# Kernel optimization log

Hardware: AMD Instinct MI355X
Metric: run time of the kernel (lower is better)

## Reference

```python
import jax, jax.numpy as jnp
import numpy as np

B, S, H, I, E, TOPK = 2, 2048, 1024, 2048, 8, 2


def setup_inputs() -> dict:
    key = jax.random.key(0)
    k0, k1, k2, k3, k4 = jax.random.split(key, 5)
    return {
        "hidden_state": jax.random.normal(k0, (B, S, H), dtype=jnp.float32),
        "gate_w": jax.random.normal(k1, (H, E), dtype=jnp.float32) * 0.02,
        "Wg": jax.random.normal(k2, (E, H, I), dtype=jnp.float32) * 0.02,
        "Wu": jax.random.normal(k3, (E, H, I), dtype=jnp.float32) * 0.02,
        "Wd": jax.random.normal(k4, (E, I, H), dtype=jnp.float32) * 0.02,
        "top_k": TOPK,
    }


def reference(hidden_state, gate_w, Wg, Wu, Wd, top_k):
    b, s, h = hidden_state.shape
    x = hidden_state.reshape(-1, h)                      # [T, H]
    T = x.shape[0]
    router_logits = x @ gate_w                           # [T, E]
    probs = jax.nn.softmax(router_logits, axis=-1)
    top_p, top_i = jax.lax.top_k(probs, top_k)           # [T, K]
    # norm_expert=False -> no renormalization of top-k probs
    # scatter top-k probs into dense per-expert combine weights [T, E]
    weights = jnp.zeros((T, probs.shape[-1]), dtype=x.dtype)
    weights = weights.at[jnp.arange(T)[:, None], top_i].add(top_p)
    # dense per-expert SwiGLU MLP (equivalent math to gather/scatter dispatch)
    g = jnp.einsum('th,ehi->tei', x, Wg)                 # [T, E, I]
    u = jnp.einsum('th,ehi->tei', x, Wu)
    mid = jax.nn.silu(g) * u
    expert_out = jnp.einsum('tei,eih->teh', mid, Wd)     # [T, E, H]
    final = jnp.einsum('te,teh->th', weights, expert_out)
    return final.reshape(b, s, h), router_logits
```

## Files before the change

### kernel.cpp

```cpp
#include <hip/hip_runtime.h>
#include <stdint.h>
#include <math.h>

#define T_TOK 4096
#define H_DIM 1024
#define I_DIM 2048
#define E_NUM 8
#define PMAX (T_TOK * 2 + E_NUM * 128)

#define WCONV_BLOCKS (E_NUM * 512 * 3)
#define ROUTER_BLOCKS (T_TOK / 4)

typedef __attribute__((ext_vector_type(8))) short short8;
typedef __attribute__((ext_vector_type(4))) float f32x4;
typedef unsigned short u16;
typedef unsigned int u32;

__device__ __forceinline__ u16 f2bf(float f) {
  union { float f; u32 u; } v; v.f = f;
  u32 r = v.u + 0x7fffu + ((v.u >> 16) & 1u);
  return (u16)(r >> 16);
}
__device__ __forceinline__ float bf2f(u16 a) {
  union { u32 u; float f; } v; v.u = ((u32)a) << 16; return v.f;
}

__device__ __forceinline__ void async_ld16(const u16* g, u16* l) {
  __builtin_amdgcn_global_load_lds(
      (const __attribute__((address_space(1))) void*)g,
      (__attribute__((address_space(3))) void*)l, 16, 0, 0);
}

__global__ void front_kernel(const float* __restrict__ Wg, const float* __restrict__ Wu,
                             const float* __restrict__ Wd, u16* __restrict__ wgt,
                             u16* __restrict__ wut, u16* __restrict__ wdt,
                             const float* __restrict__ x, u16* __restrict__ xb,
                             const float* __restrict__ gw, float* __restrict__ logits_out,
                             int* __restrict__ te, float* __restrict__ tw) {
  __shared__ float sgw[E_NUM * H_DIM];
  const int b = blockIdx.x;
  if (b < WCONV_BLOCKS) {
    const int zz = b / (E_NUM * 512);
    const int idx = b - zz * (E_NUM * 512);
    const float* src = (zz == 0) ? Wg : (zz == 1) ? Wu : Wd;
    u16* dst = (zz == 0) ? wgt : (zz == 1) ? wut : wdt;
    const int R = (zz == 2) ? I_DIM : H_DIM;
    const int C = (zz == 2) ? H_DIM : I_DIM;
    const int cpt = C >> 6;
    const int e = idx >> 9;
    const int ti = idx & 511;
    const int r0 = (ti / cpt) << 6;
    const int c0 = (ti % cpt) << 6;
    const float* s = src + (size_t)e * H_DIM * I_DIM;
    u16* d = dst + (size_t)e * H_DIM * I_DIM;

    const int wave = threadIdx.x >> 6, lane = threadIdx.x & 63;
    const int g = lane >> 4, lq = lane & 15;
    const int c = c0 + wave * 16 + g * 4;
    const int r = r0 + lq * 4;

    float4 v0 = *(const float4*)(s + (size_t)(r + 0) * C + c);
    float4 v1 = *(const float4*)(s + (size_t)(r + 1) * C + c);
    float4 v2 = *(const float4*)(s + (size_t)(r + 2) * C + c);
    float4 v3 = *(const float4*)(s + (size_t)(r + 3) * C + c);

    ushort4 o;
    o.x = f2bf(v0.x); o.y = f2bf(v1.x); o.z = f2bf(v2.x); o.w = f2bf(v3.x);
    *(ushort4*)(d + (size_t)(c + 0) * R + r) = o;
    o.x = f2bf(v0.y); o.y = f2bf(v1.y); o.z = f2bf(v2.y); o.w = f2bf(v3.y);
    *(ushort4*)(d + (size_t)(c + 1) * R + r) = o;
    o.x = f2bf(v0.z); o.y = f2bf(v1.z); o.z = f2bf(v2.z); o.w = f2bf(v3.z);
    *(ushort4*)(d + (size_t)(c + 2) * R + r) = o;
    o.x = f2bf(v0.w); o.y = f2bf(v1.w); o.z = f2bf(v2.w); o.w = f2bf(v3.w);
    *(ushort4*)(d + (size_t)(c + 3) * R + r) = o;
  } else {
    const int rb = b - WCONV_BLOCKS;
    for (int j = threadIdx.x; j < (H_DIM * E_NUM) / 4; j += 256) {
      float4 v = ((const float4*)gw)[j];
      int base = j * 4;
      sgw[((base + 0) & 7) * H_DIM + ((base + 0) >> 3)] = v.x;
      sgw[((base + 1) & 7) * H_DIM + ((base + 1) >> 3)] = v.y;
      sgw[((base + 2) & 7) * H_DIM + ((base + 2) >> 3)] = v.z;
      sgw[((base + 3) & 7) * H_DIM + ((base + 3) >> 3)] = v.w;
    }
    __syncthreads();
    const int wave = threadIdx.x >> 6, lane = threadIdx.x & 63;
    const int t = rb * 4 + wave;
    const float* xr = x + (size_t)t * H_DIM;
    u16* xbr = xb + (size_t)t * H_DIM;
    float acc[8];
#pragma unroll
    for (int e = 0; e < 8; e++) acc[e] = 0.f;
#pragma unroll
    for (int it = 0; it < 4; it++) {
      int h0 = it * 256 + lane * 4;
      float4 xv = *(const float4*)(xr + h0);
      ushort4 o;
      o.x = f2bf(xv.x); o.y = f2bf(xv.y); o.z = f2bf(xv.z); o.w = f2bf(xv.w);
      *(ushort4*)(xbr + h0) = o;
#pragma unroll
      for (int e = 0; e < 8; e++) {
        float4 g = *(const float4*)(&sgw[e * H_DIM + h0]);
        acc[e] += xv.x * g.x + xv.y * g.y + xv.z * g.z + xv.w * g.w;
      }
    }
#pragma unroll
    for (int m = 1; m < 64; m <<= 1) {
#pragma unroll
      for (int e = 0; e < 8; e++) acc[e] += __shfl_xor(acc[e], m, 64);
    }
    if (lane == 0) {
      float mx = acc[0];
#pragma unroll
      for (int e = 1; e < 8; e++) mx = fmaxf(mx, acc[e]);
      float p[8]; float s = 0.f;
#pragma unroll
      for (int e = 0; e < 8; e++) { p[e] = __expf(acc[e] - mx); s += p[e]; }
      float inv = 1.0f / s;
      int e0 = 0; float b0 = acc[0];
#pragma unroll
      for (int e = 1; e < 8; e++) if (acc[e] > b0) { b0 = acc[e]; e0 = e; }
      int e1 = -1; float b1 = -1e30f;
#pragma unroll
      for (int e = 0; e < 8; e++) if (e != e0 && acc[e] > b1) { b1 = acc[e]; e1 = e; }
#pragma unroll
      for (int e = 0; e < 8; e++) logits_out[(size_t)t * 8 + e] = acc[e];
      te[t * 2] = e0; te[t * 2 + 1] = e1;
      tw[t * 2] = p[e0] * inv; tw[t * 2 + 1] = p[e1] * inv;
    }
  }
}

__global__ __launch_bounds__(1024) void sort_kernel(const int* __restrict__ te,
                                                    int* __restrict__ offs,
                                                    int* __restrict__ token_list,
                                                    int* __restrict__ tpos) {
  __shared__ int wsum[16][8];
  __shared__ int wbase[16][8];
  __shared__ int soffs[9];
  const int tid = threadIdx.x;
  const int wave = tid >> 6, lane = tid & 63;

  for (int j = tid; j < PMAX; j += 1024) token_list[j] = 0;

  const int t0 = tid * 4;
  int e_loc[8];
  int cnt[8];
#pragma unroll
  for (int e = 0; e < 8; e++) cnt[e] = 0;
#pragma unroll
  for (int k = 0; k < 8; k++) {
    int e = te[t0 * 2 + k];
    e_loc[k] = e;
    cnt[e]++;
  }
  int excl[8];
#pragma unroll
  for (int e = 0; e < 8; e++) {
    int v = cnt[e];
    int s = v;
#pragma unroll
    for (int d = 1; d < 64; d <<= 1) {
      int u = __shfl_up(s, d, 64);
      if (lane >= d) s += u;
    }
    excl[e] = s - v;
    if (lane == 63) wsum[wave][e] = s;
  }
  __syncthreads();
  if (tid < 8) {
    int e = tid;
    int a = 0;
    for (int w2 = 0; w2 < 16; w2++) { wbase[w2][e] = a; a += wsum[w2][e]; }
    wsum[0][e] = a;
  }
  __syncthreads();
  if (tid == 0) {
    int a = 0;
    for (int e = 0; e < 8; e++) {
      soffs[e] = a;
      a += (wsum[0][e] + 127) & ~127;
    }
    soffs[8] = a;
    for (int e = 0; e <= 8; e++) offs[e] = soffs[e];
  }
  __syncthreads();
  int base[8];
#pragma unroll
  for (int e = 0; e < 8; e++) base[e] = soffs[e] + wbase[wave][e] + excl[e];
#pragma unroll
  for (int k = 0; k < 8; k++) {
    int e = e_loc[k];
    int pos = base[e]++;
    int t = t0 + (k >> 1);
    token_list[pos] = t;
    tpos[t * 2 + (k & 1)] = pos;
  }
}

#define BK1 64

__global__ __launch_bounds__(256, 2) void gemm1_kernel(
    const u16* __restrict__ xb, const u16* __restrict__ wgt, const u16* __restrict__ wut,
    const int* __restrict__ token_list, const int* __restrict__ offs, u16* __restrict__ mid) {
  const int e = blockIdx.z;
  const int off = offs[e];
  const int pcount = offs[e + 1] - off;
  const int row0 = blockIdx.y * 128;
  if (row0 >= pcount) return;
  const int n0 = blockIdx.x * 128;

  __shared__ __align__(16) u16 As[128 * BK1];
  __shared__ __align__(16) u16 Bg[128 * BK1];
  __shared__ __align__(16) u16 Bu[128 * BK1];

  const int tid = threadIdx.x;
  const int wave = tid >> 6, lane = tid & 63;
  const int wm = (wave >> 1) * 64, wn = (wave & 1) * 64;
  const int quad = lane >> 4, lr = lane & 15;
  const int l7 = lr & 7;

  f32x4 accg[4][4], accu[4][4];
  f32x4 z = {0.f, 0.f, 0.f, 0.f};
#pragma unroll
  for (int i = 0; i < 4; i++)
#pragma unroll
    for (int j = 0; j < 4; j++) { accg[i][j] = z; accu[i][j] = z; }

  const u16* wgb = wgt + (size_t)e * I_DIM * H_DIM;
  const u16* wub = wut + (size_t)e * I_DIM * H_DIM;

  const u16* ga[4]; const u16* gg[4]; const u16* gu[4];
  u16 *la[4], *lg[4], *lu[4];
#pragma unroll
  for (int i = 0; i < 4; i++) {
    int c = tid + 256 * i;
    int row = c >> 3, kcl = c & 7;
    int kg = kcl ^ (row & 7);
    int tok = token_list[off + row0 + row];
    ga[i] = xb + (size_t)tok * H_DIM + kg * 8;
    gg[i] = wgb + (size_t)(n0 + row) * H_DIM + kg * 8;
    gu[i] = wub + (size_t)(n0 + row) * H_DIM + kg * 8;
    la[i] = &As[c * 8]; lg[i] = &Bg[c * 8]; lu[i] = &Bu[c * 8];
  }

  for (int kt = 0; kt < H_DIM / BK1; kt++) {
    const int k0 = kt * BK1;
#pragma unroll
    for (int i = 0; i < 4; i++) {
      async_ld16(ga[i] + k0, la[i]);
      async_ld16(gg[i] + k0, lg[i]);
      async_ld16(gu[i] + k0, lu[i]);
    }
    __syncthreads();
#pragma unroll
    for (int kk = 0; kk < 2; kk++) {
      const int slot = ((kk << 2) + quad) ^ l7;
      short8 af[4];
#pragma unroll
      for (int im = 0; im < 4; im++)
        af[im] = *(const short8*)(&As[(wm + im * 16 + lr) * BK1 + slot * 8]);
#pragma unroll
      for (int in = 0; in < 4; in++) {
        short8 bg = *(const short8*)(&Bg[(wn + in * 16 + lr) * BK1 + slot * 8]);
        short8 bu = *(const short8*)(&Bu[(wn + in * 16 + lr) * BK1 + slot * 8]);
#pragma unroll
        for (int im = 0; im < 4; im++) {
          accg[im][in] = __builtin_amdgcn_mfma_f32_16x16x32_bf16(af[im], bg, accg[im][in], 0, 0, 0);
          accu[im][in] = __builtin_amdgcn_mfma_f32_16x16x32_bf16(af[im], bu, accu[im][in], 0, 0, 0);
        }
      }
    }
    __syncthreads();
  }

#pragma unroll
  for (int im = 0; im < 4; im++) {
#pragma unroll
    for (int r = 0; r < 4; r++) {
      int row = row0 + wm + im * 16 + quad * 4 + r;
      u16* mrow = mid + (size_t)(off + row) * I_DIM + n0 + wn;
#pragma unroll
      for (int in = 0; in < 4; in++) {
        float g = accg[im][in][r];
        float u = accu[im][in][r];
        float sv = g / (1.0f + __expf(-g)) * u;
        mrow[in * 16 + lr] = f2bf(sv);
      }
    }
  }
}

__global__ __launch_bounds__(256, 2) void gemm2_kernel(
    const u16* __restrict__ mid, const u16* __restrict__ wdt,
    const int* __restrict__ offs, u16* __restrict__ eout) {
  const int e = blockIdx.z;
  const int off = offs[e];
  const int pcount = offs[e + 1] - off;
  const int row0 = blockIdx.y * 128;
  if (row0 >= pcount) return;
  const int n0 = blockIdx.x * 128;

  __shared__ __align__(16) u16 As[128 * BK1];
  __shared__ __align__(16) u16 Bs[128 * BK1];

  const int tid = threadIdx.x;
  const int wave = tid >> 6, lane = tid & 63;
  const int wm = (wave >> 1) * 64, wn = (wave & 1) * 64;
  const int quad = lane >> 4, lr = lane & 15;
  const int l7 = lr & 7;

  f32x4 acc[4][4];
  f32x4 z = {0.f, 0.f, 0.f, 0.f};
#pragma unroll
  for (int i = 0; i < 4; i++)
#pragma unroll
    for (int j = 0; j < 4; j++) acc[i][j] = z;

  const u16* wdb = wdt + (size_t)e * H_DIM * I_DIM;

  const u16* ga[4]; const u16* gb[4];
  u16 *la[4], *lb[4];
#pragma unroll
  for (int i = 0; i < 4; i++) {
    int c = tid + 256 * i;
    int row = c >> 3, kcl = c & 7;
    int kg = kcl ^ (row & 7);
    ga[i] = mid + (size_t)(off + row0 + row) * I_DIM + kg * 8;
    gb[i] = wdb + (size_t)(n0 + row) * I_DIM + kg * 8;
    la[i] = &As[c * 8]; lb[i] = &Bs[c * 8];
  }

  for (int kt = 0; kt < I_DIM / BK1; kt++) {
    const int k0 = kt * BK1;
#pragma unroll
    for (int i = 0; i < 4; i++) {
      async_ld16(ga[i] + k0, la[i]);
      async_ld16(gb[i] + k0, lb[i]);
    }
    __syncthreads();
#pragma unroll
    for (int kk = 0; kk < 2; kk++) {
      const int slot = ((kk << 2) + quad) ^ l7;
      short8 af[4];
#pragma unroll
      for (int im = 0; im < 4; im++)
        af[im] = *(const short8*)(&As[(wm + im * 16 + lr) * BK1 + slot * 8]);
#pragma unroll
      for (int in = 0; in < 4; in++) {
        short8 bf = *(const short8*)(&Bs[(wn + in * 16 + lr) * BK1 + slot * 8]);
#pragma unroll
        for (int im = 0; im < 4; im++)
          acc[im][in] = __builtin_amdgcn_mfma_f32_16x16x32_bf16(af[im], bf, acc[im][in], 0, 0, 0);
      }
    }
    __syncthreads();
  }

#pragma unroll
  for (int im = 0; im < 4; im++) {
#pragma unroll
    for (int r = 0; r < 4; r++) {
      int row = row0 + wm + im * 16 + quad * 4 + r;
      u16* orow = eout + (size_t)(off + row) * H_DIM + n0 + wn;
#pragma unroll
      for (int in = 0; in < 4; in++)
        orow[in * 16 + lr] = f2bf(acc[im][in][r]);
    }
  }
}

__global__ void combine_kernel(const u16* __restrict__ eout, const int* __restrict__ tpos,
                               const float* __restrict__ tw, float* __restrict__ out) {
  const int half = threadIdx.x >> 7;
  const int t = blockIdx.x * 2 + half;
  const int lt = threadIdx.x & 127;
  const int h0 = lt * 8;
  const int p0 = tpos[t * 2], p1 = tpos[t * 2 + 1];
  const float w0 = tw[t * 2], w1 = tw[t * 2 + 1];
  ushort4 a0 = *(const ushort4*)(eout + (size_t)p0 * H_DIM + h0);
  ushort4 a1 = *(const ushort4*)(eout + (size_t)p0 * H_DIM + h0 + 4);
  ushort4 b0 = *(const ushort4*)(eout + (size_t)p1 * H_DIM + h0);
  ushort4 b1 = *(const ushort4*)(eout + (size_t)p1 * H_DIM + h0 + 4);
  float4 o0, o1;
  o0.x = w0 * bf2f(a0.x) + w1 * bf2f(b0.x);
  o0.y = w0 * bf2f(a0.y) + w1 * bf2f(b0.y);
  o0.z = w0 * bf2f(a0.z) + w1 * bf2f(b0.z);
  o0.w = w0 * bf2f(a0.w) + w1 * bf2f(b0.w);
  o1.x = w0 * bf2f(a1.x) + w1 * bf2f(b1.x);
  o1.y = w0 * bf2f(a1.y) + w1 * bf2f(b1.y);
  o1.z = w0 * bf2f(a1.z) + w1 * bf2f(b1.z);
  o1.w = w0 * bf2f(a1.w) + w1 * bf2f(b1.w);
  float* orow = out + (size_t)t * H_DIM + h0;
  *(float4*)(orow) = o0;
  *(float4*)(orow + 4) = o1;
}

extern "C" void kernel_launch(void* const* d_in, const int* in_sizes, int n_in,
                              void* d_out, int out_size, void* d_ws, size_t ws_size,
                              hipStream_t stream) {
  const float* x  = (const float*)d_in[0];
  const float* gw = (const float*)d_in[1];
  const float* Wg = (const float*)d_in[2];
  const float* Wu = (const float*)d_in[3];
  const float* Wd = (const float*)d_in[4];
  float* out = (float*)d_out;
  float* out_logits = out + (size_t)T_TOK * H_DIM;

  char* w = (char*)d_ws;
  size_t o = 0;
  auto take = [&](size_t bytes) { char* p = w + o; o += (bytes + 255) & ~(size_t)255; return p; };
  int*   offs        = (int*)take((E_NUM + 1) * 4);
  int*   te          = (int*)take((size_t)T_TOK * 2 * 4);
  float* tw          = (float*)take((size_t)T_TOK * 2 * 4);
  int*   token_list  = (int*)take((size_t)PMAX * 4);
  int*   tpos        = (int*)take((size_t)T_TOK * 2 * 4);
  u16*   xb          = (u16*)take((size_t)T_TOK * H_DIM * 2);
  u16*   wgt         = (u16*)take((size_t)E_NUM * H_DIM * I_DIM * 2);
  u16*   wut         = (u16*)take((size_t)E_NUM * H_DIM * I_DIM * 2);
  u16*   wdt         = (u16*)take((size_t)E_NUM * H_DIM * I_DIM * 2);
  u16*   mid         = (u16*)take((size_t)PMAX * I_DIM * 2);
  u16*   eout        = wgt;
  (void)in_sizes; (void)n_in; (void)out_size; (void)ws_size;

  front_kernel<<<WCONV_BLOCKS + ROUTER_BLOCKS, 256, 0, stream>>>(
      Wg, Wu, Wd, wgt, wut, wdt, x, xb, gw, out_logits, te, tw);
  sort_kernel<<<1, 1024, 0, stream>>>(te, offs, token_list, tpos);
  gemm1_kernel<<<dim3(I_DIM / 128, PMAX / 128, E_NUM), 256, 0, stream>>>(xb, wgt, wut, token_list, offs, mid);
  gemm2_kernel<<<dim3(H_DIM / 128, PMAX / 128, E_NUM), 256, 0, stream>>>(mid, wdt, offs, eout);
  combine_kernel<<<T_TOK / 2, 256, 0, stream>>>(eout, tpos, tw, out);
}
```

Measured before the change: 406.3 us.

## Switch expert GEMMs to 32x32x16 MFMA and a flattened padded-row grid

Both grouped GEMM kernels now use the 32x32x16 bf16 MFMA with 2x2 fragments per wave instead of 4x4 fragments of 16x16x32. This halves the LDS fragment reads per MFMA and changes the register layout of the epilogue. The launch grid is flattened from a 3D per-expert grid to a 1D grid over padded global row tiles, with the expert found by scanning the offsets. Far fewer blocks launch only to exit early. The epilogue stores become strided row writes of 32 lanes, which may coalesce less well.

```diff
diff --git a/kernel.cpp b/kernel.cpp
--- a/kernel.cpp
+++ b/kernel.cpp
@@ -12,7 +12,7 @@
 #define ROUTER_BLOCKS (T_TOK / 4)
 
 typedef __attribute__((ext_vector_type(8))) short short8;
-typedef __attribute__((ext_vector_type(4))) float f32x4;
+typedef __attribute__((ext_vector_type(16))) float f32x16;
 typedef unsigned short u16;
 typedef unsigned int u32;
 
@@ -203,12 +203,13 @@
 __global__ __launch_bounds__(256, 2) void gemm1_kernel(
     const u16* __restrict__ xb, const u16* __restrict__ wgt, const u16* __restrict__ wut,
     const int* __restrict__ token_list, const int* __restrict__ offs, u16* __restrict__ mid) {
-  const int e = blockIdx.z;
-  const int off = offs[e];
-  const int pcount = offs[e + 1] - off;
-  const int row0 = blockIdx.y * 128;
-  if (row0 >= pcount) return;
-  const int n0 = blockIdx.x * 128;
+  const int bid = blockIdx.x;
+  const int my = bid >> 4, nx = bid & 15;
+  const int grow0 = my * 128;
+  if (grow0 >= offs[E_NUM]) return;
+  int e = 0;
+  while (offs[e + 1] <= grow0) e++;
+  const int n0 = nx * 128;
 
   __shared__ __align__(16) u16 As[128 * BK1];
   __shared__ __align__(16) u16 Bg[128 * BK1];
@@ -217,15 +218,16 @@
   const int tid = threadIdx.x;
   const int wave = tid >> 6, lane = tid & 63;
   const int wm = (wave >> 1) * 64, wn = (wave & 1) * 64;
-  const int quad = lane >> 4, lr = lane & 15;
-  const int l7 = lr & 7;
-
-  f32x4 accg[4][4], accu[4][4];
-  f32x4 z = {0.f, 0.f, 0.f, 0.f};
-#pragma unroll
-  for (int i = 0; i < 4; i++)
-#pragma unroll
-    for (int j = 0; j < 4; j++) { accg[i][j] = z; accu[i][j] = z; }
+  const int l31 = lane & 31, kh = lane >> 5;
+
+  f32x16 accg[2][2], accu[2][2];
+#pragma unroll
+  for (int i = 0; i < 2; i++)
+#pragma unroll
+    for (int j = 0; j < 2; j++) {
+      accg[i][j] = (f32x16)(0.f);
+      accu[i][j] = (f32x16)(0.f);
+    }
 
   const u16* wgb = wgt + (size_t)e * I_DIM * H_DIM;
   const u16* wub = wut + (size_t)e * I_DIM * H_DIM;
@@ -237,7 +239,7 @@
     int c = tid + 256 * i;
     int row = c >> 3, kcl = c & 7;
     int kg = kcl ^ (row & 7);
-    int tok = token_list[off + row0 + row];
+    int tok = token_list[grow0 + row];
     ga[i] = xb + (size_t)tok * H_DIM + kg * 8;
     gg[i] = wgb + (size_t)(n0 + row) * H_DIM + kg * 8;
     gu[i] = wub + (size_t)(n0 + row) * H_DIM + kg * 8;
@@ -254,52 +256,58 @@
     }
     __syncthreads();
 #pragma unroll
-    for (int kk = 0; kk < 2; kk++) {
-      const int slot = ((kk << 2) + quad) ^ l7;
-      short8 af[4];
-#pragma unroll
-      for (int im = 0; im < 4; im++)
-        af[im] = *(const short8*)(&As[(wm + im * 16 + lr) * BK1 + slot * 8]);
-#pragma unroll
-      for (int in = 0; in < 4; in++) {
-        short8 bg = *(const short8*)(&Bg[(wn + in * 16 + lr) * BK1 + slot * 8]);
-        short8 bu = *(const short8*)(&Bu[(wn + in * 16 + lr) * BK1 + slot * 8]);
-#pragma unroll
-        for (int im = 0; im < 4; im++) {
-          accg[im][in] = __builtin_amdgcn_mfma_f32_16x16x32_bf16(af[im], bg, accg[im][in], 0, 0, 0);
-          accu[im][in] = __builtin_amdgcn_mfma_f32_16x16x32_bf16(af[im], bu, accu[im][in], 0, 0, 0);
+    for (int ks = 0; ks < 4; ks++) {
+      const int lc = ks * 2 + kh;
+      short8 af[2], bgf[2], buf2[2];
+#pragma unroll
+      for (int mb = 0; mb < 2; mb++) {
+        int row = wm + mb * 32 + l31;
+        af[mb] = *(const short8*)(&As[row * BK1 + (lc ^ (row & 7)) * 8]);
+      }
+#pragma unroll
+      for (int nb = 0; nb < 2; nb++) {
+        int row = wn + nb * 32 + l31;
+        int sl = (lc ^ (row & 7)) * 8;
+        bgf[nb] = *(const short8*)(&Bg[row * BK1 + sl]);
+        buf2[nb] = *(const short8*)(&Bu[row * BK1 + sl]);
+      }
+#pragma unroll
+      for (int mb = 0; mb < 2; mb++)
+#pragma unroll
+        for (int nb = 0; nb < 2; nb++) {
+          accg[mb][nb] = __builtin_amdgcn_mfma_f32_32x32x16_bf16(af[mb], bgf[nb], accg[mb][nb], 0, 0, 0);
+          accu[mb][nb] = __builtin_amdgcn_mfma_f32_32x32x16_bf16(af[mb], buf2[nb], accu[mb][nb], 0, 0, 0);
         }
-      }
     }
     __syncthreads();
   }
 
 #pragma unroll
-  for (int im = 0; im < 4; im++) {
-#pragma unroll
-    for (int r = 0; r < 4; r++) {
-      int row = row0 + wm + im * 16 + quad * 4 + r;
-      u16* mrow = mid + (size_t)(off + row) * I_DIM + n0 + wn;
-#pragma unroll
-      for (int in = 0; in < 4; in++) {
-        float g = accg[im][in][r];
-        float u = accu[im][in][r];
+  for (int mb = 0; mb < 2; mb++)
+#pragma unroll
+    for (int nb = 0; nb < 2; nb++) {
+      u16* base = mid + (size_t)(grow0 + wm + mb * 32 + 4 * kh) * I_DIM + n0 + wn + nb * 32 + l31;
+#pragma unroll
+      for (int reg = 0; reg < 16; reg++) {
+        int dr = (reg & 3) + 8 * (reg >> 2);
+        float g = accg[mb][nb][reg];
+        float u = accu[mb][nb][reg];
         float sv = g / (1.0f + __expf(-g)) * u;
-        mrow[in * 16 + lr] = f2bf(sv);
-      }
-    }
-  }
+        base[(size_t)dr * I_DIM] = f2bf(sv);
+      }
+    }
 }
 
 __global__ __launch_bounds__(256, 2) void gemm2_kernel(
     const u16* __restrict__ mid, const u16* __restrict__ wdt,
     const int* __restrict__ offs, u16* __restrict__ eout) {
-  const int e = blockIdx.z;
-  const int off = offs[e];
-  const int pcount = offs[e + 1] - off;
-  const int row0 = blockIdx.y * 128;
-  if (row0 >= pcount) return;
-  const int n0 = blockIdx.x * 128;
+  const int bid = blockIdx.x;
+  const int my = bid >> 3, nx = bid & 7;
+  const int grow0 = my * 128;
+  if (grow0 >= offs[E_NUM]) return;
+  int e = 0;
+  while (offs[e + 1] <= grow0) e++;
+  const int n0 = nx * 128;
 
   __shared__ __align__(16) u16 As[128 * BK1];
   __shared__ __align__(16) u16 Bs[128 * BK1];
@@ -307,15 +315,13 @@
   const int tid = threadIdx.x;
   const int wave = tid >> 6, lane = tid & 63;
   const int wm = (wave >> 1) * 64, wn = (wave & 1) * 64;
-  const int quad = lane >> 4, lr = lane & 15;
-  const int l7 = lr & 7;
-
-  f32x4 acc[4][4];
-  f32x4 z = {0.f, 0.f, 0.f, 0.f};
-#pragma unroll
-  for (int i = 0; i < 4; i++)
-#pragma unroll
-    for (int j = 0; j < 4; j++) acc[i][j] = z;
+  const int l31 = lane & 31, kh = lane >> 5;
+
+  f32x16 acc[2][2];
+#pragma unroll
+  for (int i = 0; i < 2; i++)
+#pragma unroll
+    for (int j = 0; j < 2; j++) acc[i][j] = (f32x16)(0.f);
 
   const u16* wdb = wdt + (size_t)e * H_DIM * I_DIM;
 
@@ -326,7 +332,7 @@
     int c = tid + 256 * i;
     int row = c >> 3, kcl = c & 7;
     int kg = kcl ^ (row & 7);
-    ga[i] = mid + (size_t)(off + row0 + row) * I_DIM + kg * 8;
+    ga[i] = mid + (size_t)(grow0 + row) * I_DIM + kg * 8;
     gb[i] = wdb + (size_t)(n0 + row) * I_DIM + kg * 8;
     la[i] = &As[c * 8]; lb[i] = &Bs[c * 8];
   }
@@ -340,34 +346,39 @@
     }
     __syncthreads();
 #pragma unroll
-    for (int kk = 0; kk < 2; kk++) {
-      const int slot = ((kk << 2) + quad) ^ l7;
-      short8 af[4];
-#pragma unroll
-      for (int im = 0; im < 4; im++)
-        af[im] = *(const short8*)(&As[(wm + im * 16 + lr) * BK1 + slot * 8]);
-#pragma unroll
-      for (int in = 0; in < 4; in++) {
-        short8 bf = *(const short8*)(&Bs[(wn + in * 16 + lr) * BK1 + slot * 8]);
-#pragma unroll
-        for (int im = 0; im < 4; im++)
-          acc[im][in] = __builtin_amdgcn_mfma_f32_16x16x32_bf16(af[im], bf, acc[im][in], 0, 0, 0);
-      }
+    for (int ks = 0; ks < 4; ks++) {
+      const int lc = ks * 2 + kh;
+      short8 af[2], bf[2];
+#pragma unroll
+      for (int mb = 0; mb < 2; mb++) {
+        int row = wm + mb * 32 + l31;
+        af[mb] = *(const short8*)(&As[row * BK1 + (lc ^ (row & 7)) * 8]);
+      }
+#pragma unroll
+      for (int nb = 0; nb < 2; nb++) {
+        int row = wn + nb * 32 + l31;
+        bf[nb] = *(const short8*)(&Bs[row * BK1 + (lc ^ (row & 7)) * 8]);
+      }
+#pragma unroll
+      for (int mb = 0; mb < 2; mb++)
+#pragma unroll
+        for (int nb = 0; nb < 2; nb++)
+          acc[mb][nb] = __builtin_amdgcn_mfma_f32_32x32x16_bf16(af[mb], bf[nb], acc[mb][nb], 0, 0, 0);
     }
     __syncthreads();
   }
 
 #pragma unroll
-  for (int im = 0; im < 4; im++) {
-#pragma unroll
-    for (int r = 0; r < 4; r++) {
-      int row = row0 + wm + im * 16 + quad * 4 + r;
-      u16* orow = eout + (size_t)(off + row) * H_DIM + n0 + wn;
-#pragma unroll
-      for (int in = 0; in < 4; in++)
-        orow[in * 16 + lr] = f2bf(acc[im][in][r]);
-    }
-  }
+  for (int mb = 0; mb < 2; mb++)
+#pragma unroll
+    for (int nb = 0; nb < 2; nb++) {
+      u16* base = eout + (size_t)(grow0 + wm + mb * 32 + 4 * kh) * H_DIM + n0 + wn + nb * 32 + l31;
+#pragma unroll
+      for (int reg = 0; reg < 16; reg++) {
+        int dr = (reg & 3) + 8 * (reg >> 2);
+        base[(size_t)dr * H_DIM] = f2bf(acc[mb][nb][reg]);
+      }
+    }
 }
 
 __global__ void combine_kernel(const u16* __restrict__ eout, const int* __restrict__ tpos,
@@ -426,7 +437,7 @@
   front_kernel<<<WCONV_BLOCKS + ROUTER_BLOCKS, 256, 0, stream>>>(
       Wg, Wu, Wd, wgt, wut, wdt, x, xb, gw, out_logits, te, tw);
   sort_kernel<<<1, 1024, 0, stream>>>(te, offs, token_list, tpos);
-  gemm1_kernel<<<dim3(I_DIM / 128, PMAX / 128, E_NUM), 256, 0, stream>>>(xb, wgt, wut, token_list, offs, mid);
-  gemm2_kernel<<<dim3(H_DIM / 128, PMAX / 128, E_NUM), 256, 0, stream>>>(mid, wdt, offs, eout);
+  gemm1_kernel<<<(PMAX / 128) * (I_DIM / 128), 256, 0, stream>>>(xb, wgt, wut, token_list, offs, mid);
+  gemm2_kernel<<<(PMAX / 128) * (H_DIM / 128), 256, 0, stream>>>(mid, wdt, offs, eout);
   combine_kernel<<<T_TOK / 2, 256, 0, stream>>>(eout, tpos, tw, out);
 }
```

Measured after the change: 406.3 us. About the same (-0.0%).
